# Kernel optimization log

Measured on AMD Instinct MI355X. Metric: run time of the kernel, lower is better.

Reference implementation:

```python
import jax, jax.numpy as jnp
import numpy as np

B, IN, H, OUT = 256, 512, 1024, 512
S, Wd, SH = 512, 256, 3          # memory_slots, memory_width, shift_range
P_READ = Wd + 2 + SH + 1         # key, beta, gate, shift(3), gamma
P_WRITE = P_READ + 2 * Wd        # + erase, add


def setup_inputs() -> dict:
    key = jax.random.key(0)
    ks = jax.random.split(key, 8)
    sc = 0.02
    return {
        "x": jax.random.normal(ks[0], (B, IN), jnp.float32),
        "W_ih": jax.random.normal(ks[1], (4 * H, IN + Wd), jnp.float32) * sc,
        "b_ih": jnp.zeros((4 * H,), jnp.float32),
        "W_hh": jax.random.normal(ks[2], (4 * H, H), jnp.float32) * sc,
        "b_hh": jnp.zeros((4 * H,), jnp.float32),
        "W_read": jax.random.normal(ks[3], (P_READ, H), jnp.float32) * sc,
        "b_read": jnp.zeros((P_READ,), jnp.float32),
        "W_write": jax.random.normal(ks[4], (P_WRITE, H), jnp.float32) * sc,
        "b_write": jnp.zeros((P_WRITE,), jnp.float32),
        "W_out": jax.random.normal(ks[5], (OUT, H + Wd), jnp.float32) * sc,
        "b_out": jnp.zeros((OUT,), jnp.float32),
        "mem_bias": jax.random.normal(ks[6], (S, Wd), jnp.float32) * sc,
    }


def _content_address(key_v, beta, memory):
    # cosine similarity of key [B,Wd] vs memory [B,S,Wd], eps=1e-8 like torch
    num = jnp.einsum('bw,bsw->bs', key_v, memory)
    kn = jnp.maximum(jnp.linalg.norm(key_v, axis=1, keepdims=True), 1e-8)
    mn = jnp.maximum(jnp.linalg.norm(memory, axis=2), 1e-8)
    sim = num / (kn * mn) * beta[:, None]
    return jax.nn.softmax(sim, axis=1)


def _address(p, prev_w, memory):
    # content_and_location addressing for a single head
    key_v = p[:, :Wd]
    beta = jax.nn.softplus(p[:, Wd])
    gate = jax.nn.sigmoid(p[:, Wd + 1])
    shift = jax.nn.softmax(p[:, Wd + 2:Wd + 2 + SH], axis=1)
    gamma = 1.0 + jax.nn.softplus(p[:, Wd + 2 + SH])
    cw = _content_address(key_v, beta, memory)
    g = gate[:, None]
    gw = g * cw + (1.0 - g) * prev_w  # interpolation gate
    # circular shift: shifted[pos] = s0*w[pos-1] + s1*w[pos] + s2*w[pos+1]
    sw = (shift[:, 0:1] * jnp.roll(gw, 1, axis=1)
          + shift[:, 1:2] * gw
          + shift[:, 2:3] * jnp.roll(gw, -1, axis=1))
    sp = sw ** gamma[:, None]  # sharpening
    return sp / (jnp.sum(sp, axis=1, keepdims=True) + 1e-6)


def reference(x, W_ih, b_ih, W_hh, b_hh, W_read, b_read, W_write, b_write, W_out, b_out, mem_bias):
    Bb = x.shape[0]
    # init_state (prev_state=None path)
    memory = jnp.broadcast_to(mem_bias[None], (Bb, S, Wd))
    w0 = jnp.zeros((Bb, S), x.dtype).at[:, 0].set(1.0)
    rv = jnp.zeros((Bb, Wd), x.dtype)
    h = jnp.zeros((Bb, H), x.dtype)
    c = jnp.zeros((Bb, H), x.dtype)
    # LSTMCell controller
    inp = jnp.concatenate([x, rv], axis=1)
    gates = inp @ W_ih.T + b_ih + h @ W_hh.T + b_hh
    i, f, g, o = jnp.split(gates, 4, axis=1)
    c = jax.nn.sigmoid(f) * c + jax.nn.sigmoid(i) * jnp.tanh(g)
    h = jax.nn.sigmoid(o) * jnp.tanh(c)
    # read head addressing (1 head)
    rp = h @ W_read.T + b_read
    read_w = _address(rp, w0, memory)
    # write head addressing + erase/add (1 head)
    wp = h @ W_write.T + b_write
    write_w = _address(wp, w0, memory)
    erase = jax.nn.sigmoid(wp[:, P_READ:P_READ + Wd])
    add = jnp.tanh(wp[:, P_READ + Wd:])
    memory = memory * (1.0 - write_w[:, :, None] * erase[:, None, :]) + write_w[:, :, None] * add[:, None, :]
    # read after write
    rv = jnp.einsum('bsw,bs->bw', memory, read_w)
    out = jnp.concatenate([h, rv], axis=1) @ W_out.T + b_out
    return out
```

## Files before the change

### kernel.cpp

```cpp
#include <hip/hip_runtime.h>
#include <hip/hip_bf16.h>
#include <math.h>

#define BB   256
#define INW  512
#define HH   1024
#define OUTW 512
#define SS   512
#define WD   256
#define P_READ  262
#define P_WRITE 774
#define RW_LD   1056
#define W_OFF   272

typedef __attribute__((ext_vector_type(8))) short bf16x8;
typedef __attribute__((ext_vector_type(4))) float f32x4;

__device__ __forceinline__ float sigmoidf(float x) { return 1.f / (1.f + expf(-x)); }
__device__ __forceinline__ float softplusf(float x) { return (x > 20.f) ? x : log1pf(expf(x)); }
__device__ __forceinline__ unsigned short f2b(float f) {
    union { float f; unsigned u; } c; c.f = f;
    return (unsigned short)((c.u + 0x7FFFu + ((c.u >> 16) & 1u)) >> 16);
}
__device__ __forceinline__ void st_bf4(__hip_bfloat16* d, float a, float b, float c, float e) {
    ushort4 u; u.x = f2b(a); u.y = f2b(b); u.z = f2b(c); u.w = f2b(e);
    *reinterpret_cast<ushort4*>(d) = u;
}
__device__ __forceinline__ float wave_sum(float v) {
    #pragma unroll
    for (int off = 32; off > 0; off >>= 1) v += __shfl_down(v, off, 64);
    return v;
}

#define N_WIH (3072*512)
#define N_WRW (RW_LD*1024)
#define N_WO  (512*1280)
#define N_X   (256*512)
#define N_MB  (512*256)
#define N_MT  (256*512)
#define N_BIA 3072
#define N_BRW RW_LD
#define N_TOT (N_WIH+N_WRW+N_WO+N_X+N_MB+N_MT+N_BIA+N_BRW)
#define NB_CVT ((N_TOT/4 + 255) / 256)

__global__ __launch_bounds__(256)
void convert_all(const float* __restrict__ W_ih, const float* __restrict__ b_ih,
                 const float* __restrict__ b_hh,
                 const float* __restrict__ W_read, const float* __restrict__ b_read,
                 const float* __restrict__ W_write, const float* __restrict__ b_write,
                 const float* __restrict__ W_out, const float* __restrict__ x,
                 const float* __restrict__ mem,
                 __hip_bfloat16* __restrict__ Wih_c, __hip_bfloat16* __restrict__ Wrw_p,
                 __hip_bfloat16* __restrict__ Wo_b, __hip_bfloat16* __restrict__ x_b,
                 __hip_bfloat16* __restrict__ mem_b, __hip_bfloat16* __restrict__ memT_b,
                 float* __restrict__ bias_c, float* __restrict__ bias_rw,
                 float* __restrict__ mem_norm)
{
    if (blockIdx.x >= NB_CVT) {
        __shared__ float red[4];
        int s = blockIdx.x - NB_CVT;
        float v = mem[(size_t)s * WD + threadIdx.x];
        float vv = wave_sum(v * v);
        if ((threadIdx.x & 63) == 0) red[threadIdx.x >> 6] = vv;
        __syncthreads();
        if (threadIdx.x == 0)
            mem_norm[s] = fmaxf(sqrtf(red[0] + red[1] + red[2] + red[3]), 1e-8f);
        return;
    }
    long i = ((long)blockIdx.x * 256 + threadIdx.x) * 4;
    if (i >= N_TOT) return;
    if (i < N_WIH) {
        int r = (int)(i >> 9), c = (int)(i & 511);
        int sr = r < 1024 ? r : r + 1024;
        float4 v = *reinterpret_cast<const float4*>(W_ih + (size_t)sr * 768 + c);
        st_bf4(Wih_c + i, v.x, v.y, v.z, v.w);
        return;
    }
    i -= N_WIH;
    if (i < N_WRW) {
        int r = (int)(i >> 10), c = (int)(i & 1023);
        float4 v = make_float4(0.f, 0.f, 0.f, 0.f);
        if (r < W_OFF) { if (r < P_READ) v = *reinterpret_cast<const float4*>(W_read + (size_t)r * 1024 + c); }
        else { int wr = r - W_OFF; if (wr < P_WRITE) v = *reinterpret_cast<const float4*>(W_write + (size_t)wr * 1024 + c); }
        st_bf4(Wrw_p + i, v.x, v.y, v.z, v.w);
        return;
    }
    i -= N_WRW;
    if (i < N_WO) {
        float4 v = *reinterpret_cast<const float4*>(W_out + i);
        st_bf4(Wo_b + i, v.x, v.y, v.z, v.w);
        return;
    }
    i -= N_WO;
    if (i < N_X) {
        float4 v = *reinterpret_cast<const float4*>(x + i);
        st_bf4(x_b + i, v.x, v.y, v.z, v.w);
        return;
    }
    i -= N_X;
    if (i < N_MB) {
        float4 v = *reinterpret_cast<const float4*>(mem + i);
        st_bf4(mem_b + i, v.x, v.y, v.z, v.w);
        return;
    }
    i -= N_MB;
    if (i < N_MT) {
        int w = (int)(i >> 9), s = (int)(i & 511);
        st_bf4(memT_b + i, mem[(size_t)s * 256 + w], mem[(size_t)(s + 1) * 256 + w],
               mem[(size_t)(s + 2) * 256 + w], mem[(size_t)(s + 3) * 256 + w]);
        return;
    }
    i -= N_MT;
    if (i < N_BIA) {
        #pragma unroll
        for (int u = 0; u < 4; ++u) {
            long r = i + u;
            long sr = r < 1024 ? r : r + 1024;
            bias_c[r] = b_ih[sr] + b_hh[sr];
        }
        return;
    }
    i -= N_BIA;
    {
        #pragma unroll
        for (int u = 0; u < 4; ++u) {
            long r = i + u;
            float v = 0.f;
            if (r < W_OFF) { if (r < P_READ) v = b_read[r]; }
            else { long wr = r - W_OFF; if (wr < P_WRITE) v = b_write[wr]; }
            bias_rw[r] = v;
        }
    }
}

__global__ __launch_bounds__(64)
void gemm_gates(const __hip_bfloat16* __restrict__ x_b,
                const __hip_bfloat16* __restrict__ Wih_c,
                const float* __restrict__ bias_c,
                __hip_bfloat16* __restrict__ h_b)
{
    const int l = threadIdx.x;
    const int bn = blockIdx.x * 16;
    const int bm = blockIdx.y * 16;
    const int r = l & 15, q = l >> 4;
    const __hip_bfloat16* ap = x_b + (size_t)(bm + r) * INW + q * 8;
    const __hip_bfloat16* bi = Wih_c + (size_t)(bn + r) * INW + q * 8;
    const __hip_bfloat16* bg = bi + (size_t)1024 * INW;
    const __hip_bfloat16* bo = bi + (size_t)2048 * INW;
    f32x4 ai = {0.f,0.f,0.f,0.f}, ag = ai, ao = ai;
    #pragma unroll
    for (int k = 0; k < INW; k += 32) {
        bf16x8 a = *reinterpret_cast<const bf16x8*>(ap + k);
        ai = __builtin_amdgcn_mfma_f32_16x16x32_bf16(a, *reinterpret_cast<const bf16x8*>(bi + k), ai, 0, 0, 0);
        ag = __builtin_amdgcn_mfma_f32_16x16x32_bf16(a, *reinterpret_cast<const bf16x8*>(bg + k), ag, 0, 0, 0);
        ao = __builtin_amdgcn_mfma_f32_16x16x32_bf16(a, *reinterpret_cast<const bf16x8*>(bo + k), ao, 0, 0, 0);
    }
    const int j = bn + r;
    const float bii = bias_c[j], big = bias_c[1024 + j], bio = bias_c[2048 + j];
    #pragma unroll
    for (int jj = 0; jj < 4; ++jj) {
        int b = bm + q * 4 + jj;
        float c = sigmoidf(ai[jj] + bii) * tanhf(ag[jj] + big);
        h_b[(size_t)b * HH + j] = __float2bfloat16(sigmoidf(ao[jj] + bio) * tanhf(c));
    }
}

__global__ __launch_bounds__(64)
void gemm_dual(const __hip_bfloat16* __restrict__ h_b,
               const __hip_bfloat16* __restrict__ Wrw_p,
               const __hip_bfloat16* __restrict__ Wo_b,
               const float* __restrict__ bias_rw, const float* __restrict__ b_out,
               float* __restrict__ rpwp, float* __restrict__ out,
               __hip_bfloat16* __restrict__ keys)
{
    const int bid = blockIdx.x;
    const int lane = threadIdx.x;
    const int r = lane & 15, q = lane >> 4;
    int bm, bn, ldb;
    const __hip_bfloat16* B;
    if (bid < 1056) { int nt = bid % 66, mt = bid / 66; bm = mt * 16; bn = nt * 16; B = Wrw_p; ldb = HH; }
    else { int o = bid - 1056; int nt = o & 31, mt = o >> 5; bm = mt * 16; bn = nt * 16; B = Wo_b; ldb = 1280; }

    const __hip_bfloat16* ap = h_b + (size_t)(bm + r) * HH + q * 8;
    const __hip_bfloat16* bp = B + (size_t)(bn + r) * ldb + q * 8;
    f32x4 a0 = {0.f,0.f,0.f,0.f}, a1 = a0;
    #pragma unroll 8
    for (int k = 0; k < 512; k += 32) {
        a0 = __builtin_amdgcn_mfma_f32_16x16x32_bf16(
            *reinterpret_cast<const bf16x8*>(ap + k),
            *reinterpret_cast<const bf16x8*>(bp + k), a0, 0, 0, 0);
        a1 = __builtin_amdgcn_mfma_f32_16x16x32_bf16(
            *reinterpret_cast<const bf16x8*>(ap + 512 + k),
            *reinterpret_cast<const bf16x8*>(bp + 512 + k), a1, 0, 0, 0);
    }
    const int col = bn + r;
    if (bid < 1056) {
        const float bv = bias_rw[col];
        #pragma unroll
        for (int j = 0; j < 4; ++j) {
            int m = bm + q * 4 + j;
            float v = a0[j] + a1[j] + bv;
            rpwp[(size_t)m * RW_LD + col] = v;
            if (col < WD)
                keys[(size_t)m * WD + col] = __float2bfloat16(v);
            else if (col >= W_OFF && col < W_OFF + WD)
                keys[(size_t)(256 + m) * WD + (col - W_OFF)] = __float2bfloat16(v);
        }
    } else {
        const float bv = b_out[col];
        #pragma unroll
        for (int j = 0; j < 4; ++j) {
            int m = bm + q * 4 + j;
            out[(size_t)m * OUTW + col] = a0[j] + a1[j] + bv;
        }
    }
}

__global__ __launch_bounds__(64)
void gemm_num(const __hip_bfloat16* __restrict__ keys,
              const __hip_bfloat16* __restrict__ mem_b,
              const float* __restrict__ mem_norm,
              float* __restrict__ numd)
{
    const int l = threadIdx.x;
    const int bn = blockIdx.x * 16;
    const int bm = blockIdx.y * 16;
    const int r = l & 15, q = l >> 4;
    const __hip_bfloat16* ap = keys + (size_t)(bm + r) * WD + q * 8;
    const __hip_bfloat16* bp = mem_b + (size_t)(bn + r) * WD + q * 8;
    f32x4 acc = {0.f,0.f,0.f,0.f};
    #pragma unroll
    for (int k = 0; k < WD; k += 32)
        acc = __builtin_amdgcn_mfma_f32_16x16x32_bf16(
            *reinterpret_cast<const bf16x8*>(ap + k),
            *reinterpret_cast<const bf16x8*>(bp + k), acc, 0, 0, 0);
    const int col = bn + r;
    const float inv = 1.f / mem_norm[col];
    #pragma unroll
    for (int j = 0; j < 4; ++j)
        numd[(size_t)(bm + q * 4 + j) * SS + col] = acc[j] * inv;
}

__device__ __forceinline__ void redpair_sum(float& a, float& b, volatile float* redA, volatile float* redB) {
    #pragma unroll
    for (int off = 32; off > 0; off >>= 1) { a += __shfl_down(a, off, 64); b += __shfl_down(b, off, 64); }
    int wid = threadIdx.x >> 6;
    __syncthreads();
    if ((threadIdx.x & 63) == 0) { redA[wid] = a; redB[wid] = b; }
    __syncthreads();
    a = redA[0]+redA[1]+redA[2]+redA[3]+redA[4]+redA[5]+redA[6]+redA[7];
    b = redB[0]+redB[1]+redB[2]+redB[3]+redB[4]+redB[5]+redB[6]+redB[7];
}
__device__ __forceinline__ void redpair_max(float& a, float& b, volatile float* redA, volatile float* redB) {
    #pragma unroll
    for (int off = 32; off > 0; off >>= 1) { a = fmaxf(a, __shfl_down(a, off, 64)); b = fmaxf(b, __shfl_down(b, off, 64)); }
    int wid = threadIdx.x >> 6;
    __syncthreads();
    if ((threadIdx.x & 63) == 0) { redA[wid] = a; redB[wid] = b; }
    __syncthreads();
    a = fmaxf(fmaxf(fmaxf(redA[0],redA[1]),fmaxf(redA[2],redA[3])),fmaxf(fmaxf(redA[4],redA[5]),fmaxf(redA[6],redA[7])));
    b = fmaxf(fmaxf(fmaxf(redB[0],redB[1]),fmaxf(redB[2],redB[3])),fmaxf(fmaxf(redB[4],redB[5]),fmaxf(redB[6],redB[7])));
}

__global__ __launch_bounds__(512)
void address_fused(const float* __restrict__ rpwp, const float* __restrict__ numd,
                   __hip_bfloat16* __restrict__ A12, float* __restrict__ t3)
{
    const int b = blockIdx.x;
    const int t = threadIdx.x;
    const float* pr = rpwp + (size_t)b * RW_LD;
    const float* pw = pr + W_OFF;

    __shared__ float redA[8], redB[8];
    __shared__ float bufr[SS], bufw[SS];

    float beta_r  = softplusf(pr[WD]);
    float gate_r  = sigmoidf(pr[WD + 1]);
    float r0 = pr[WD+2], r1 = pr[WD+3], r2 = pr[WD+4];
    float rmx = fmaxf(r0, fmaxf(r1, r2));
    float re0 = expf(r0-rmx), re1 = expf(r1-rmx), re2 = expf(r2-rmx);
    float rinv = 1.f / (re0+re1+re2);
    float shr0 = re0*rinv, shr1 = re1*rinv, shr2 = re2*rinv;
    float gamma_r = 1.f + softplusf(pr[WD + 5]);

    float beta_w  = softplusf(pw[WD]);
    float gate_w  = sigmoidf(pw[WD + 1]);
    float w0 = pw[WD+2], w1 = pw[WD+3], w2 = pw[WD+4];
    float wmx = fmaxf(w0, fmaxf(w1, w2));
    float we0 = expf(w0-wmx), we1 = expf(w1-wmx), we2 = expf(w2-wmx);
    float winv = 1.f / (we0+we1+we2);
    float shw0 = we0*winv, shw1 = we1*winv, shw2 = we2*winv;
    float gamma_w = 1.f + softplusf(pw[WD + 5]);

    {
        float kv = (t < WD) ? pr[t] : pw[t - WD];
        float vv = kv * kv;
        #pragma unroll
        for (int off = 32; off > 0; off >>= 1) vv += __shfl_down(vv, off, 64);
        int wid = t >> 6;
        if ((t & 63) == 0) redA[wid] = vv;
        __syncthreads();
    }
    float knr = fmaxf(sqrtf(redA[0]+redA[1]+redA[2]+redA[3]), 1e-8f);
    float knw = fmaxf(sqrtf(redA[4]+redA[5]+redA[6]+redA[7]), 1e-8f);
    __syncthreads();

    float sim_r = numd[(size_t)b * SS + t]         / knr * beta_r;
    float sim_w = numd[(size_t)(256 + b) * SS + t] / knw * beta_w;

    float mr = sim_r, mw = sim_w;
    redpair_max(mr, mw, redA, redB);
    float exr = expf(sim_r - mr), exw = expf(sim_w - mw);
    float sr = exr, sw = exw;
    redpair_sum(sr, sw, redA, redB);
    float cwr = exr / sr, cww = exw / sw;

    float onehot = (t == 0) ? 1.f : 0.f;
    float gwr = gate_r * cwr + (1.f - gate_r) * onehot;
    float gww = gate_w * cww + (1.f - gate_w) * onehot;
    __syncthreads();
    bufr[t] = gwr; bufw[t] = gww;
    __syncthreads();

    int tm = (t + SS - 1) & (SS - 1), tp = (t + 1) & (SS - 1);
    float swr = shr0 * bufr[tm] + shr1 * gwr + shr2 * bufr[tp];
    float sww = shw0 * bufw[tm] + shw1 * gww + shw2 * bufw[tp];

    float spr = powf(fmaxf(swr, 0.f), gamma_r), spw = powf(fmaxf(sww, 0.f), gamma_w);
    float ssr = spr, ssw = spw;
    redpair_sum(ssr, ssw, redA, redB);
    float rfin = spr / (ssr + 1e-6f);
    float wfin = spw / (ssw + 1e-6f);

    float prod = rfin * wfin;
    A12[(size_t)b * SS + t] = __float2bfloat16(rfin);
    A12[(size_t)(256 + b) * SS + t] = __float2bfloat16(prod);
    float tp3 = prod, dummy = 0.f;
    redpair_sum(tp3, dummy, redA, redB);
    if (t == 0) t3[b] = tp3;
}

__global__ __launch_bounds__(64)
void gemm_t12rv(const __hip_bfloat16* __restrict__ A12,
                const __hip_bfloat16* __restrict__ memT_b,
                const float* __restrict__ rpwp, const float* __restrict__ t3,
                __hip_bfloat16* __restrict__ rv_b)
{
    const int l = threadIdx.x;
    const int bn = blockIdx.x * 16;
    const int bm = blockIdx.y * 16;
    const int r = l & 15, q = l >> 4;
    const __hip_bfloat16* a1 = A12 + (size_t)(bm + r) * SS + q * 8;
    const __hip_bfloat16* a2 = a1 + (size_t)256 * SS;
    const __hip_bfloat16* bp = memT_b + (size_t)(bn + r) * SS + q * 8;
    f32x4 acc1 = {0.f,0.f,0.f,0.f}, acc2 = acc1;
    #pragma unroll
    for (int k = 0; k < SS; k += 32) {
        bf16x8 bb = *reinterpret_cast<const bf16x8*>(bp + k);
        acc1 = __builtin_amdgcn_mfma_f32_16x16x32_bf16(*reinterpret_cast<const bf16x8*>(a1 + k), bb, acc1, 0, 0, 0);
        acc2 = __builtin_amdgcn_mfma_f32_16x16x32_bf16(*reinterpret_cast<const bf16x8*>(a2 + k), bb, acc2, 0, 0, 0);
    }
    const int w = bn + r;
    #pragma unroll
    for (int j = 0; j < 4; ++j) {
        int b = bm + q * 4 + j;
        const float* row = rpwp + (size_t)b * RW_LD;
        float e = sigmoidf(row[W_OFF + P_READ + w]);
        float a = tanhf(row[W_OFF + P_READ + WD + w]);
        float rv = acc1[j] - e * acc2[j] + a * t3[b];
        rv_b[(size_t)b * WD + w] = __float2bfloat16(rv);
    }
}

__global__ __launch_bounds__(64)
void gemm_outrv(const __hip_bfloat16* __restrict__ rv_b,
                const __hip_bfloat16* __restrict__ Wo_b,
                float* __restrict__ out)
{
    const int l = threadIdx.x;
    const int bn = blockIdx.x * 16;
    const int bm = blockIdx.y * 16;
    const int r = l & 15, q = l >> 4;
    const __hip_bfloat16* ap = rv_b + (size_t)(bm + r) * WD + q * 8;
    const __hip_bfloat16* bp = Wo_b + (size_t)(bn + r) * 1280 + 1024 + q * 8;
    f32x4 acc = {0.f,0.f,0.f,0.f};
    #pragma unroll
    for (int k = 0; k < WD; k += 32)
        acc = __builtin_amdgcn_mfma_f32_16x16x32_bf16(
            *reinterpret_cast<const bf16x8*>(ap + k),
            *reinterpret_cast<const bf16x8*>(bp + k), acc, 0, 0, 0);
    const int col = bn + r;
    #pragma unroll
    for (int j = 0; j < 4; ++j) {
        int m = bm + q * 4 + j;
        out[(size_t)m * OUTW + col] += acc[j];
    }
}

extern "C" void kernel_launch(void* const* d_in, const int* in_sizes, int n_in,
                              void* d_out, int out_size, void* d_ws, size_t ws_size,
                              hipStream_t stream)
{
    const float* x       = (const float*)d_in[0];
    const float* W_ih    = (const float*)d_in[1];
    const float* b_ih    = (const float*)d_in[2];
    const float* b_hh    = (const float*)d_in[4];
    const float* W_read  = (const float*)d_in[5];
    const float* b_read  = (const float*)d_in[6];
    const float* W_write = (const float*)d_in[7];
    const float* b_write = (const float*)d_in[8];
    const float* W_out   = (const float*)d_in[9];
    const float* b_out   = (const float*)d_in[10];
    const float* mem     = (const float*)d_in[11];

    float* ws = (float*)d_ws;
    float* rpwp     = ws;
    float* numd     = ws + 270336;
    float* bias_c   = ws + 532480;
    float* bias_rw  = ws + 535552;
    float* mem_norm = ws + 536608;
    float* t3       = ws + 537120;
    __hip_bfloat16* bfb = (__hip_bfloat16*)(ws + 537376);
    __hip_bfloat16* x_b    = bfb;
    __hip_bfloat16* Wih_c  = bfb + 131072;
    __hip_bfloat16* Wrw_p  = bfb + 1703936;
    __hip_bfloat16* Wo_b   = bfb + 2785280;
    __hip_bfloat16* mem_b  = bfb + 3440640;
    __hip_bfloat16* memT_b = bfb + 3571712;
    __hip_bfloat16* h_b    = bfb + 3702784;
    __hip_bfloat16* keys   = bfb + 3964928;
    __hip_bfloat16* A12    = bfb + 4096000;
    __hip_bfloat16* rv_b   = bfb + 4358144;
    float* out = (float*)d_out;

    convert_all<<<NB_CVT + SS, 256, 0, stream>>>(
        W_ih, b_ih, b_hh, W_read, b_read, W_write, b_write, W_out, x, mem,
        Wih_c, Wrw_p, Wo_b, x_b, mem_b, memT_b, bias_c, bias_rw, mem_norm);
    gemm_gates<<<dim3(64, 16), 64, 0, stream>>>(x_b, Wih_c, bias_c, h_b);
    gemm_dual<<<1568, 64, 0, stream>>>(h_b, Wrw_p, Wo_b, bias_rw, b_out, rpwp, out, keys);
    gemm_num<<<dim3(32, 32), 64, 0, stream>>>(keys, mem_b, mem_norm, numd);
    address_fused<<<BB, 512, 0, stream>>>(rpwp, numd, A12, t3);
    gemm_t12rv<<<dim3(16, 16), 64, 0, stream>>>(A12, memT_b, rpwp, t3, rv_b);
    gemm_outrv<<<dim3(32, 16), 64, 0, stream>>>(rv_b, Wo_b, out);
}
```

Before: 59.03 us.

## Precompute memory-projected key weights to fold content similarity into controller GEMM

The key-vs-memory similarity numerator is reassociated as h·(W_key^T·memᵀ/‖m‖) plus a bias column. The precomputed weight-memory product M1ext is built alongside the gates GEMM in one stage, so the separate keys/gemm_num dependency is removed. The stage that previously computed read/write params and output now also produces numd directly, cutting one kernel launch and one serial stage. In exchange there is extra conversion work (WkT transpose) and a larger K=1056 GEMM against a 1024-wide M1 per batch, plus a bias column trick via a constant-1 column in h2.

```diff
diff --git a/kernel.cpp b/kernel.cpp
--- a/kernel.cpp
+++ b/kernel.cpp
@@ -12,19 +12,19 @@
 #define P_WRITE 774
 #define RW_LD   1056
 #define W_OFF   272
+#define H2LD 1056
+#define M1LD 1056
 
 typedef __attribute__((ext_vector_type(8))) short bf16x8;
 typedef __attribute__((ext_vector_type(4))) float f32x4;
 
 __device__ __forceinline__ float sigmoidf(float x) { return 1.f / (1.f + expf(-x)); }
 __device__ __forceinline__ float softplusf(float x) { return (x > 20.f) ? x : log1pf(expf(x)); }
-__device__ __forceinline__ unsigned short f2b(float f) {
-    union { float f; unsigned u; } c; c.f = f;
-    return (unsigned short)((c.u + 0x7FFFu + ((c.u >> 16) & 1u)) >> 16);
-}
-__device__ __forceinline__ void st_bf4(__hip_bfloat16* d, float a, float b, float c, float e) {
-    ushort4 u; u.x = f2b(a); u.y = f2b(b); u.z = f2b(c); u.w = f2b(e);
-    *reinterpret_cast<ushort4*>(d) = u;
+__device__ __forceinline__ void st_bf4f(__hip_bfloat16* d, float a, float b, float c, float e) {
+    union { ushort4 u4; __hip_bfloat16 h[4]; } u;
+    u.h[0] = __float2bfloat16(a); u.h[1] = __float2bfloat16(b);
+    u.h[2] = __float2bfloat16(c); u.h[3] = __float2bfloat16(e);
+    *reinterpret_cast<ushort4*>(d) = u.u4;
 }
 __device__ __forceinline__ float wave_sum(float v) {
     #pragma unroll
@@ -38,9 +38,10 @@
 #define N_X   (256*512)
 #define N_MB  (512*256)
 #define N_MT  (256*512)
+#define N_WKT (2*1024*256)
 #define N_BIA 3072
 #define N_BRW RW_LD
-#define N_TOT (N_WIH+N_WRW+N_WO+N_X+N_MB+N_MT+N_BIA+N_BRW)
+#define N_TOT (N_WIH+N_WRW+N_WO+N_X+N_MB+N_MT+N_WKT+N_BIA+N_BRW)
 #define NB_CVT ((N_TOT/4 + 255) / 256)
 
 __global__ __launch_bounds__(256)
@@ -53,6 +54,7 @@
                  __hip_bfloat16* __restrict__ Wih_c, __hip_bfloat16* __restrict__ Wrw_p,
                  __hip_bfloat16* __restrict__ Wo_b, __hip_bfloat16* __restrict__ x_b,
                  __hip_bfloat16* __restrict__ mem_b, __hip_bfloat16* __restrict__ memT_b,
+                 __hip_bfloat16* __restrict__ WkT,
                  float* __restrict__ bias_c, float* __restrict__ bias_rw,
                  float* __restrict__ mem_norm)
 {
@@ -73,7 +75,7 @@
         int r = (int)(i >> 9), c = (int)(i & 511);
         int sr = r < 1024 ? r : r + 1024;
         float4 v = *reinterpret_cast<const float4*>(W_ih + (size_t)sr * 768 + c);
-        st_bf4(Wih_c + i, v.x, v.y, v.z, v.w);
+        st_bf4f(Wih_c + i, v.x, v.y, v.z, v.w);
         return;
     }
     i -= N_WIH;
@@ -82,35 +84,45 @@
         float4 v = make_float4(0.f, 0.f, 0.f, 0.f);
         if (r < W_OFF) { if (r < P_READ) v = *reinterpret_cast<const float4*>(W_read + (size_t)r * 1024 + c); }
         else { int wr = r - W_OFF; if (wr < P_WRITE) v = *reinterpret_cast<const float4*>(W_write + (size_t)wr * 1024 + c); }
-        st_bf4(Wrw_p + i, v.x, v.y, v.z, v.w);
+        st_bf4f(Wrw_p + i, v.x, v.y, v.z, v.w);
         return;
     }
     i -= N_WRW;
     if (i < N_WO) {
         float4 v = *reinterpret_cast<const float4*>(W_out + i);
-        st_bf4(Wo_b + i, v.x, v.y, v.z, v.w);
+        st_bf4f(Wo_b + i, v.x, v.y, v.z, v.w);
         return;
     }
     i -= N_WO;
     if (i < N_X) {
         float4 v = *reinterpret_cast<const float4*>(x + i);
-        st_bf4(x_b + i, v.x, v.y, v.z, v.w);
+        st_bf4f(x_b + i, v.x, v.y, v.z, v.w);
         return;
     }
     i -= N_X;
     if (i < N_MB) {
         float4 v = *reinterpret_cast<const float4*>(mem + i);
-        st_bf4(mem_b + i, v.x, v.y, v.z, v.w);
+        st_bf4f(mem_b + i, v.x, v.y, v.z, v.w);
         return;
     }
     i -= N_MB;
     if (i < N_MT) {
         int w = (int)(i >> 9), s = (int)(i & 511);
-        st_bf4(memT_b + i, mem[(size_t)s * 256 + w], mem[(size_t)(s + 1) * 256 + w],
-               mem[(size_t)(s + 2) * 256 + w], mem[(size_t)(s + 3) * 256 + w]);
+        st_bf4f(memT_b + i, mem[(size_t)s * 256 + w], mem[(size_t)(s + 1) * 256 + w],
+                mem[(size_t)(s + 2) * 256 + w], mem[(size_t)(s + 3) * 256 + w]);
         return;
     }
     i -= N_MT;
+    if (i < N_WKT) {
+        int mat = (int)(i >> 18);
+        int ii = (int)(i & 262143);
+        int j = ii >> 8, w0 = ii & 255;
+        const float* src = (mat ? W_write : W_read);
+        st_bf4f(WkT + i, src[(size_t)(w0 + 0) * 1024 + j], src[(size_t)(w0 + 1) * 1024 + j],
+                src[(size_t)(w0 + 2) * 1024 + j], src[(size_t)(w0 + 3) * 1024 + j]);
+        return;
+    }
+    i -= N_WKT;
     if (i < N_BIA) {
         #pragma unroll
         for (int u = 0; u < 4; ++u) {
@@ -133,112 +145,183 @@
     }
 }
 
+#define S2_GATES 1024
+#define S2_M1    4096
+#define S2_BT    16
+#define S2_H2P   1
+#define S2_M1P   16
+#define S2_TOT   (S2_GATES + S2_M1 + S2_BT + S2_H2P + S2_M1P)
+
 __global__ __launch_bounds__(64)
-void gemm_gates(const __hip_bfloat16* __restrict__ x_b,
-                const __hip_bfloat16* __restrict__ Wih_c,
-                const float* __restrict__ bias_c,
-                __hip_bfloat16* __restrict__ h_b)
-{
-    const int l = threadIdx.x;
-    const int bn = blockIdx.x * 16;
-    const int bm = blockIdx.y * 16;
-    const int r = l & 15, q = l >> 4;
-    const __hip_bfloat16* ap = x_b + (size_t)(bm + r) * INW + q * 8;
-    const __hip_bfloat16* bi = Wih_c + (size_t)(bn + r) * INW + q * 8;
-    const __hip_bfloat16* bg = bi + (size_t)1024 * INW;
-    const __hip_bfloat16* bo = bi + (size_t)2048 * INW;
-    f32x4 ai = {0.f,0.f,0.f,0.f}, ag = ai, ao = ai;
-    #pragma unroll
-    for (int k = 0; k < INW; k += 32) {
-        bf16x8 a = *reinterpret_cast<const bf16x8*>(ap + k);
-        ai = __builtin_amdgcn_mfma_f32_16x16x32_bf16(a, *reinterpret_cast<const bf16x8*>(bi + k), ai, 0, 0, 0);
-        ag = __builtin_amdgcn_mfma_f32_16x16x32_bf16(a, *reinterpret_cast<const bf16x8*>(bg + k), ag, 0, 0, 0);
-        ao = __builtin_amdgcn_mfma_f32_16x16x32_bf16(a, *reinterpret_cast<const bf16x8*>(bo + k), ao, 0, 0, 0);
-    }
-    const int j = bn + r;
-    const float bii = bias_c[j], big = bias_c[1024 + j], bio = bias_c[2048 + j];
-    #pragma unroll
-    for (int jj = 0; jj < 4; ++jj) {
-        int b = bm + q * 4 + jj;
-        float c = sigmoidf(ai[jj] + bii) * tanhf(ag[jj] + big);
-        h_b[(size_t)b * HH + j] = __float2bfloat16(sigmoidf(ao[jj] + bio) * tanhf(c));
-    }
-}
-
-__global__ __launch_bounds__(64)
-void gemm_dual(const __hip_bfloat16* __restrict__ h_b,
-               const __hip_bfloat16* __restrict__ Wrw_p,
-               const __hip_bfloat16* __restrict__ Wo_b,
-               const float* __restrict__ bias_rw, const float* __restrict__ b_out,
-               float* __restrict__ rpwp, float* __restrict__ out,
-               __hip_bfloat16* __restrict__ keys)
+void k_stage2(const __hip_bfloat16* __restrict__ x_b,
+              const __hip_bfloat16* __restrict__ Wih_c,
+              const float* __restrict__ bias_c,
+              const __hip_bfloat16* __restrict__ mem_b,
+              const __hip_bfloat16* __restrict__ WkT,
+              const float* __restrict__ b_read, const float* __restrict__ b_write,
+              const float* __restrict__ mem_norm,
+              __hip_bfloat16* __restrict__ h2, __hip_bfloat16* __restrict__ M1ext)
 {
     const int bid = blockIdx.x;
     const int lane = threadIdx.x;
     const int r = lane & 15, q = lane >> 4;
-    int bm, bn, ldb;
-    const __hip_bfloat16* B;
-    if (bid < 1056) { int nt = bid % 66, mt = bid / 66; bm = mt * 16; bn = nt * 16; B = Wrw_p; ldb = HH; }
-    else { int o = bid - 1056; int nt = o & 31, mt = o >> 5; bm = mt * 16; bn = nt * 16; B = Wo_b; ldb = 1280; }
-
-    const __hip_bfloat16* ap = h_b + (size_t)(bm + r) * HH + q * 8;
-    const __hip_bfloat16* bp = B + (size_t)(bn + r) * ldb + q * 8;
-    f32x4 a0 = {0.f,0.f,0.f,0.f}, a1 = a0;
-    #pragma unroll 8
-    for (int k = 0; k < 512; k += 32) {
-        a0 = __builtin_amdgcn_mfma_f32_16x16x32_bf16(
-            *reinterpret_cast<const bf16x8*>(ap + k),
-            *reinterpret_cast<const bf16x8*>(bp + k), a0, 0, 0, 0);
-        a1 = __builtin_amdgcn_mfma_f32_16x16x32_bf16(
-            *reinterpret_cast<const bf16x8*>(ap + 512 + k),
-            *reinterpret_cast<const bf16x8*>(bp + 512 + k), a1, 0, 0, 0);
-    }
-    const int col = bn + r;
+
+    if (bid < S2_GATES) {
+        const int bn = (bid & 63) * 16;
+        const int bm = (bid >> 6) * 16;
+        const __hip_bfloat16* ap = x_b + (size_t)(bm + r) * INW + q * 8;
+        const __hip_bfloat16* bi = Wih_c + (size_t)(bn + r) * INW + q * 8;
+        const __hip_bfloat16* bg = bi + (size_t)1024 * INW;
+        const __hip_bfloat16* bo = bi + (size_t)2048 * INW;
+        f32x4 ai = {0.f,0.f,0.f,0.f}, ag = ai, ao = ai;
+        #pragma unroll
+        for (int k = 0; k < INW; k += 32) {
+            bf16x8 a = *reinterpret_cast<const bf16x8*>(ap + k);
+            ai = __builtin_amdgcn_mfma_f32_16x16x32_bf16(a, *reinterpret_cast<const bf16x8*>(bi + k), ai, 0, 0, 0);
+            ag = __builtin_amdgcn_mfma_f32_16x16x32_bf16(a, *reinterpret_cast<const bf16x8*>(bg + k), ag, 0, 0, 0);
+            ao = __builtin_amdgcn_mfma_f32_16x16x32_bf16(a, *reinterpret_cast<const bf16x8*>(bo + k), ao, 0, 0, 0);
+        }
+        const int j = bn + r;
+        const float bii = bias_c[j], big = bias_c[1024 + j], bio = bias_c[2048 + j];
+        #pragma unroll
+        for (int jj = 0; jj < 4; ++jj) {
+            int b = bm + q * 4 + jj;
+            float c = sigmoidf(ai[jj] + bii) * tanhf(ag[jj] + big);
+            h2[(size_t)b * H2LD + j] = __float2bfloat16(sigmoidf(ao[jj] + bio) * tanhf(c));
+        }
+        return;
+    }
+    if (bid < S2_GATES + S2_M1) {
+        int m = bid - S2_GATES;
+        int mat = m >> 11;
+        int t = m & 2047;
+        int st = t >> 6, jt = t & 63;
+        const int bm = st * 16, bn = jt * 16;
+        const __hip_bfloat16* ap = mem_b + (size_t)(bm + r) * WD + q * 8;
+        const __hip_bfloat16* bp = WkT + (size_t)(mat * 1024 + bn + r) * WD + q * 8;
+        f32x4 acc = {0.f,0.f,0.f,0.f};
+        #pragma unroll
+        for (int k = 0; k < WD; k += 32)
+            acc = __builtin_amdgcn_mfma_f32_16x16x32_bf16(
+                *reinterpret_cast<const bf16x8*>(ap + k),
+                *reinterpret_cast<const bf16x8*>(bp + k), acc, 0, 0, 0);
+        #pragma unroll
+        for (int jj = 0; jj < 4; ++jj) {
+            int srow = bm + q * 4 + jj;
+            float inv = 1.f / mem_norm[srow];
+            M1ext[(size_t)(mat * 512 + srow) * M1LD + bn + r] = __float2bfloat16(acc[jj] * inv);
+        }
+        return;
+    }
+    if (bid < S2_GATES + S2_M1 + S2_BT) {
+        int gid = (bid - S2_GATES - S2_M1) * 64 + lane;
+        int mat = gid >> 9, s = gid & 511;
+        const float* bias = mat ? b_write : b_read;
+        const __hip_bfloat16* mrow = mem_b + (size_t)s * WD;
+        float acc = 0.f;
+        #pragma unroll 8
+        for (int w = 0; w < WD; ++w)
+            acc += __bfloat162float(mrow[w]) * bias[w];
+        M1ext[(size_t)gid * M1LD + 1024] = __float2bfloat16(acc / mem_norm[s]);
+        return;
+    }
+    if (bid < S2_GATES + S2_M1 + S2_BT + S2_H2P) {
+        for (int idx = lane; idx < 256 * 32; idx += 64) {
+            int row = idx >> 5, c = idx & 31;
+            h2[(size_t)row * H2LD + 1024 + c] = __float2bfloat16(c == 0 ? 1.f : 0.f);
+        }
+        return;
+    }
+    {
+        int row = (bid - (S2_GATES + S2_M1 + S2_BT + S2_H2P)) * 64 + lane;
+        #pragma unroll
+        for (int c = 1025; c < 1056; ++c)
+            M1ext[(size_t)row * M1LD + c] = __float2bfloat16(0.f);
+    }
+}
+
+__global__ __launch_bounds__(64)
+void k_stage3(const __hip_bfloat16* __restrict__ h2,
+              const __hip_bfloat16* __restrict__ Wrw_p,
+              const __hip_bfloat16* __restrict__ Wo_b,
+              const __hip_bfloat16* __restrict__ M1ext,
+              const float* __restrict__ bias_rw, const float* __restrict__ b_out,
+              float* __restrict__ rpwp, float* __restrict__ out,
+              float* __restrict__ numd)
+{
+    const int bid = blockIdx.x;
+    const int lane = threadIdx.x;
+    const int r = lane & 15, q = lane >> 4;
+
     if (bid < 1056) {
+        const int nt = bid % 66, mt = bid / 66;
+        const int bm = mt * 16, bn = nt * 16;
+        const __hip_bfloat16* ap = h2 + (size_t)(bm + r) * H2LD + q * 8;
+        const __hip_bfloat16* bp = Wrw_p + (size_t)(bn + r) * HH + q * 8;
+        f32x4 a0 = {0.f,0.f,0.f,0.f}, a1 = a0;
+        #pragma unroll 8
+        for (int k = 0; k < 512; k += 32) {
+            a0 = __builtin_amdgcn_mfma_f32_16x16x32_bf16(
+                *reinterpret_cast<const bf16x8*>(ap + k),
+                *reinterpret_cast<const bf16x8*>(bp + k), a0, 0, 0, 0);
+            a1 = __builtin_amdgcn_mfma_f32_16x16x32_bf16(
+                *reinterpret_cast<const bf16x8*>(ap + 512 + k),
+                *reinterpret_cast<const bf16x8*>(bp + 512 + k), a1, 0, 0, 0);
+        }
+        const int col = bn + r;
         const float bv = bias_rw[col];
         #pragma unroll
         for (int j = 0; j < 4; ++j) {
             int m = bm + q * 4 + j;
-            float v = a0[j] + a1[j] + bv;
-            rpwp[(size_t)m * RW_LD + col] = v;
-            if (col < WD)
-                keys[(size_t)m * WD + col] = __float2bfloat16(v);
-            else if (col >= W_OFF && col < W_OFF + WD)
-                keys[(size_t)(256 + m) * WD + (col - W_OFF)] = __float2bfloat16(v);
-        }
-    } else {
+            rpwp[(size_t)m * RW_LD + col] = a0[j] + a1[j] + bv;
+        }
+    } else if (bid < 1568) {
+        const int o = bid - 1056;
+        const int nt = o & 31, mt = o >> 5;
+        const int bm = mt * 16, bn = nt * 16;
+        const __hip_bfloat16* ap = h2 + (size_t)(bm + r) * H2LD + q * 8;
+        const __hip_bfloat16* bp = Wo_b + (size_t)(bn + r) * 1280 + q * 8;
+        f32x4 a0 = {0.f,0.f,0.f,0.f}, a1 = a0;
+        #pragma unroll 8
+        for (int k = 0; k < 512; k += 32) {
+            a0 = __builtin_amdgcn_mfma_f32_16x16x32_bf16(
+                *reinterpret_cast<const bf16x8*>(ap + k),
+                *reinterpret_cast<const bf16x8*>(bp + k), a0, 0, 0, 0);
+            a1 = __builtin_amdgcn_mfma_f32_16x16x32_bf16(
+                *reinterpret_cast<const bf16x8*>(ap + 512 + k),
+                *reinterpret_cast<const bf16x8*>(bp + 512 + k), a1, 0, 0, 0);
+        }
+        const int col = bn + r;
         const float bv = b_out[col];
         #pragma unroll
         for (int j = 0; j < 4; ++j) {
             int m = bm + q * 4 + j;
             out[(size_t)m * OUTW + col] = a0[j] + a1[j] + bv;
         }
-    }
-}
-
-__global__ __launch_bounds__(64)
-void gemm_num(const __hip_bfloat16* __restrict__ keys,
-              const __hip_bfloat16* __restrict__ mem_b,
-              const float* __restrict__ mem_norm,
-              float* __restrict__ numd)
-{
-    const int l = threadIdx.x;
-    const int bn = blockIdx.x * 16;
-    const int bm = blockIdx.y * 16;
-    const int r = l & 15, q = l >> 4;
-    const __hip_bfloat16* ap = keys + (size_t)(bm + r) * WD + q * 8;
-    const __hip_bfloat16* bp = mem_b + (size_t)(bn + r) * WD + q * 8;
-    f32x4 acc = {0.f,0.f,0.f,0.f};
-    #pragma unroll
-    for (int k = 0; k < WD; k += 32)
-        acc = __builtin_amdgcn_mfma_f32_16x16x32_bf16(
-            *reinterpret_cast<const bf16x8*>(ap + k),
-            *reinterpret_cast<const bf16x8*>(bp + k), acc, 0, 0, 0);
-    const int col = bn + r;
-    const float inv = 1.f / mem_norm[col];
-    #pragma unroll
-    for (int j = 0; j < 4; ++j)
-        numd[(size_t)(bm + q * 4 + j) * SS + col] = acc[j] * inv;
+    } else {
+        const int o = bid - 1568;
+        const int nt = o & 63, mt = o >> 6;
+        const int bm = mt * 16, bn = nt * 16;
+        const __hip_bfloat16* ap = h2 + (size_t)(bm + r) * H2LD + q * 8;
+        const __hip_bfloat16* bp = M1ext + (size_t)(bn + r) * M1LD + q * 8;
+        f32x4 a0 = {0.f,0.f,0.f,0.f}, a1 = a0;
+        #pragma unroll 8
+        for (int k = 0; k < 512; k += 32)
+            a0 = __builtin_amdgcn_mfma_f32_16x16x32_bf16(
+                *reinterpret_cast<const bf16x8*>(ap + k),
+                *reinterpret_cast<const bf16x8*>(bp + k), a0, 0, 0, 0);
+        #pragma unroll
+        for (int k = 512; k < 1056; k += 32)
+            a1 = __builtin_amdgcn_mfma_f32_16x16x32_bf16(
+                *reinterpret_cast<const bf16x8*>(ap + k),
+                *reinterpret_cast<const bf16x8*>(bp + k), a1, 0, 0, 0);
+        const int col = bn + r;
+        #pragma unroll
+        for (int j = 0; j < 4; ++j) {
+            int m = bm + q * 4 + j;
+            numd[(size_t)m * 1024 + col] = a0[j] + a1[j];
+        }
+    }
 }
 
 __device__ __forceinline__ void redpair_sum(float& a, float& b, volatile float* redA, volatile float* redB) {
@@ -305,8 +388,8 @@
     float knw = fmaxf(sqrtf(redA[4]+redA[5]+redA[6]+redA[7]), 1e-8f);
     __syncthreads();
 
-    float sim_r = numd[(size_t)b * SS + t]         / knr * beta_r;
-    float sim_w = numd[(size_t)(256 + b) * SS + t] / knw * beta_w;
+    float sim_r = numd[(size_t)b * 1024 + t]       / knr * beta_r;
+    float sim_w = numd[(size_t)b * 1024 + 512 + t] / knw * beta_w;
 
     float mr = sim_r, mw = sim_w;
     redpair_max(mr, mw, redA, redB);
@@ -416,10 +499,10 @@
     float* ws = (float*)d_ws;
     float* rpwp     = ws;
     float* numd     = ws + 270336;
-    float* bias_c   = ws + 532480;
-    float* bias_rw  = ws + 535552;
-    float* mem_norm = ws + 536608;
-    float* t3       = ws + 537120;
+    float* t3       = ws + 532480;
+    float* mem_norm = ws + 532736;
+    float* bias_c   = ws + 533248;
+    float* bias_rw  = ws + 536320;
     __hip_bfloat16* bfb = (__hip_bfloat16*)(ws + 537376);
     __hip_bfloat16* x_b    = bfb;
     __hip_bfloat16* Wih_c  = bfb + 131072;
@@ -427,18 +510,20 @@
     __hip_bfloat16* Wo_b   = bfb + 2785280;
     __hip_bfloat16* mem_b  = bfb + 3440640;
     __hip_bfloat16* memT_b = bfb + 3571712;
-    __hip_bfloat16* h_b    = bfb + 3702784;
-    __hip_bfloat16* keys   = bfb + 3964928;
-    __hip_bfloat16* A12    = bfb + 4096000;
-    __hip_bfloat16* rv_b   = bfb + 4358144;
+    __hip_bfloat16* WkT    = bfb + 3702784;
+    __hip_bfloat16* h2     = bfb + 4227072;
+    __hip_bfloat16* M1ext  = bfb + 4497408;
+    __hip_bfloat16* A12    = bfb + 5578752;
+    __hip_bfloat16* rv_b   = bfb + 5840896;
     float* out = (float*)d_out;
 
     convert_all<<<NB_CVT + SS, 256, 0, stream>>>(
         W_ih, b_ih, b_hh, W_read, b_read, W_write, b_write, W_out, x, mem,
-        Wih_c, Wrw_p, Wo_b, x_b, mem_b, memT_b, bias_c, bias_rw, mem_norm);
-    gemm_gates<<<dim3(64, 16), 64, 0, stream>>>(x_b, Wih_c, bias_c, h_b);
-    gemm_dual<<<1568, 64, 0, stream>>>(h_b, Wrw_p, Wo_b, bias_rw, b_out, rpwp, out, keys);
-    gemm_num<<<dim3(32, 32), 64, 0, stream>>>(keys, mem_b, mem_norm, numd);
+        Wih_c, Wrw_p, Wo_b, x_b, mem_b, memT_b, WkT, bias_c, bias_rw, mem_norm);
+    k_stage2<<<S2_TOT, 64, 0, stream>>>(x_b, Wih_c, bias_c, mem_b, WkT,
+                                        b_read, b_write, mem_norm, h2, M1ext);
+    k_stage3<<<2592, 64, 0, stream>>>(h2, Wrw_p, Wo_b, M1ext, bias_rw, b_out,
+                                      rpwp, out, numd);
     address_fused<<<BB, 512, 0, stream>>>(rpwp, numd, A12, t3);
     gemm_t12rv<<<dim3(16, 16), 64, 0, stream>>>(A12, memT_b, rpwp, t3, rv_b);
     gemm_outrv<<<dim3(32, 16), 64, 0, stream>>>(rv_b, Wo_b, out);
```

Result: slower. 70.88 us (+20.1%).
